# Kernel optimization log

Measured on AMD Instinct MI355X. Metric: run time of the kernel, lower is better.

The kernel has to match this reference:

```python
import jax, jax.numpy as jnp
import numpy as np

N_NODES = 50000
E = 800000
D = 64
H = 128


def _ln(x, g, b, eps=1e-5):
    m = x.mean(-1, keepdims=True)
    v = ((x - m) ** 2).mean(-1, keepdims=True)
    return (x - m) * jax.lax.rsqrt(v + eps) * g + b


def setup_inputs() -> dict:
    key = jax.random.key(0)
    ks = jax.random.split(key, 8)
    return dict(
        node_emb=jax.random.normal(ks[0], (N_NODES, D), jnp.float32),
        src=jax.random.randint(ks[1], (E,), 0, N_NODES),
        dst=jax.random.randint(ks[2], (E,), 0, N_NODES),
        noise=jax.random.uniform(ks[3], (E,), jnp.float32, 1e-6, 1.0 - 1e-6),
        W1=jax.random.normal(ks[4], (2 * D, H), jnp.float32) * 0.05,
        b1=jnp.zeros((H,), jnp.float32),
        g1=jnp.ones((H,), jnp.float32),
        bt1=jnp.zeros((H,), jnp.float32),
        W2=jax.random.normal(ks[5], (H, H // 2), jnp.float32) * 0.05,
        b2=jnp.zeros((H // 2,), jnp.float32),
        g2=jnp.ones((H // 2,), jnp.float32),
        bt2=jnp.zeros((H // 2,), jnp.float32),
        W3=jax.random.normal(ks[6], (H // 2, 1), jnp.float32) * 0.05,
        b3=jnp.zeros((1,), jnp.float32),
    )


def reference(node_emb, src, dst, noise, W1, b1, g1, bt1, W2, b2, g2, bt2, W3, b3):
    # edge gather + concat: [E, 2D]
    edge_emb = jnp.concatenate([node_emb[src], node_emb[dst]], axis=1)
    # edge MLP with LayerNorm + relu (dropout=0 / eval)
    h = jax.nn.relu(_ln(edge_emb @ W1 + b1, g1, bt1))
    h = jax.nn.relu(_ln(h @ W2 + b2, g2, bt2))
    logit = (h @ W3 + b3).reshape(-1)  # [E]
    # concrete gate, bias=0, beta=1.0 (forward default)
    beta = 1.0
    gate = jax.nn.sigmoid((jnp.log(noise) - jnp.log1p(-noise) + logit) / beta)
    # degree norm: out_deg(src)^-1/2 * in_deg(dst)^-1/2, degrees clamped to >=1
    ones = jnp.ones((src.shape[0],), node_emb.dtype)
    out_deg = jnp.maximum(jax.ops.segment_sum(ones, src, num_segments=N_NODES), 1.0)
    in_deg = jnp.maximum(jax.ops.segment_sum(ones, dst, num_segments=N_NODES), 1.0)
    norm = jax.lax.rsqrt(out_deg)[src] * jax.lax.rsqrt(in_deg)[dst]
    return gate * norm
```

## Files before the change

kernel.cpp:

```cpp
#include <hip/hip_runtime.h>
#include <hip/hip_bf16.h>

#define N_NODES 50000
#define NE      800000
#define NT32    (NE / 32)
#define NTILES  (NE / 16)

typedef __attribute__((ext_vector_type(8)))  short bf16x8;
typedef __attribute__((ext_vector_type(4)))  float f32x4;
typedef __attribute__((ext_vector_type(16))) float f32x16;
typedef __attribute__((ext_vector_type(4)))  int   i32x4;
typedef __attribute__((ext_vector_type(2)))  int   i32x2;

static __device__ __forceinline__ short f2bf(float x) {
    union { float f; unsigned u; } v; v.f = x;
    unsigned r = (v.u + 0x7fffu + ((v.u >> 16) & 1u)) >> 16;
    return (short)r;
}
static __device__ __forceinline__ float bflo(unsigned u) {
    union { unsigned u; float f; } v; v.u = u << 16; return v.f;
}
static __device__ __forceinline__ float bfhi(unsigned u) {
    union { unsigned u; float f; } v; v.u = u & 0xffff0000u; return v.f;
}
static __device__ __forceinline__ float bfs(unsigned short u) {
    union { unsigned u; float f; } v; v.u = ((unsigned)u) << 16; return v.f;
}
static __device__ __forceinline__ unsigned pk2bf(float a, float b) {
    union { __hip_bfloat162 h; unsigned u; } v;
    float2 f; f.x = a; f.y = b;
    v.h = __float22bfloat162_rn(f);
    return v.u;
}

#define OFF_W2   32768
#define OFF_B1   49152
#define OFF_B2   49408
#define OFF_GT1  49536
#define OFF_GT2  50048
#define OFF_W3   50304
#define IMG_B    50432
#define IMG_V4   (IMG_B / 16)


__global__ void prep_hist(const float* __restrict__ emb,
                          const int* __restrict__ src, const int* __restrict__ dst,
                          const float* __restrict__ W1, const float* __restrict__ b1,
                          const float* __restrict__ g1, const float* __restrict__ bt1,
                          const float* __restrict__ W2, const float* __restrict__ b2,
                          const float* __restrict__ g2, const float* __restrict__ bt2,
                          const float* __restrict__ W3,
                          ushort* __restrict__ embB, char* __restrict__ img,
                          int* __restrict__ outd, int* __restrict__ ind)
{
    const int i0 = blockIdx.x * 256 + threadIdx.x;
    const int n  = gridDim.x * 256;

    for (int t = i0; t < (N_NODES * 64 / 8); t += n) {
        const f32x4* p = (const f32x4*)(emb + (size_t)t * 8);
        f32x4 a = p[0], b = p[1];
        unsigned u0 = pk2bf(a[0], a[1]);
        unsigned u1 = pk2bf(a[2], a[3]);
        unsigned u2 = pk2bf(b[0], b[1]);
        unsigned u3 = pk2bf(b[2], b[3]);
        i32x4 o = {(int)u0, (int)u1, (int)u2, (int)u3};
        *(i32x4*)(embB + (size_t)t * 8) = o;
    }
    for (int t = i0; t < NE; t += n) {
        atomicAdd(outd + src[t], 1);
        atomicAdd(ind + dst[t], 1);
    }
    ushort* W1f = (ushort*)img;
    for (int t = i0; t < 16384; t += n) {
        int j = t & 7, lane = (t >> 3) & 63, f = t >> 9;
        int mt = f >> 3, ke = f & 7, h = lane >> 5, c = lane & 31;
        W1f[t] = f2bf(W1[(16 * ke + 8 * h + j) * 128 + 32 * mt + c]);
    }
    ushort* W2f = (ushort*)(img + OFF_W2);
    for (int t = i0; t < 8192; t += n) {
        int j = t & 7, lane = (t >> 3) & 63, f = t >> 9;
        int mt = f >> 3, ke = f & 7, h = lane >> 5, c = lane & 31;
        W2f[t] = f2bf(W2[(16 * ke + 8 * h + j) * 64 + 32 * mt + c]);
    }
    if (i0 < 128) ((ushort*)(img + OFF_B1))[i0] = f2bf(b1[i0]);
    if (i0 < 64)  ((ushort*)(img + OFF_B2))[i0] = f2bf(b2[i0]);
    if (i0 < 128) {
        int r4 = i0 & 3, h = (i0 >> 2) & 1, q4 = (i0 >> 3) & 3, mt = i0 >> 5;
        int f = 32 * mt + 8 * q4 + 4 * h + r4;
        ((unsigned*)(img + OFF_GT1))[i0] =
            (unsigned)(ushort)f2bf(g1[f]) | ((unsigned)(ushort)f2bf(bt1[f]) << 16);
    }
    if (i0 < 64) {
        int r4 = i0 & 3, h = (i0 >> 2) & 1, q4 = (i0 >> 3) & 3, mt = i0 >> 5;
        int f = 32 * mt + 8 * q4 + 4 * h + r4;
        ((unsigned*)(img + OFF_GT2))[i0] =
            (unsigned)(ushort)f2bf(g2[f]) | ((unsigned)(ushort)f2bf(bt2[f]) << 16);
        ((ushort*)(img + OFF_W3))[i0] = f2bf(W3[f]);
    }
}


__global__ __launch_bounds__(256, 3) void edge_mlp32(
    const ushort* __restrict__ embB,
    const int*   __restrict__ src, const int* __restrict__ dst,
    const float* __restrict__ noise,
    const i32x4* __restrict__ WFimg,
    const float* __restrict__ b3p,
    const int* __restrict__ outd, const int* __restrict__ ind,
    float* __restrict__ out)
{
    __shared__ i32x4 ldsv[IMG_V4];
    char* ldsb = (char*)ldsv;

    const int tid = threadIdx.x;
    for (int i = tid; i < IMG_V4; i += 256) ldsv[i] = WFimg[i];
    __syncthreads();

    const int l   = tid & 63;
    const int h   = l >> 5;
    const int c   = l & 31;

    const float b3v = b3p[0];

    bf16x8 bone = {};
    bone[0] = (h == 0) ? (short)0x3F80 : (short)0;

    const int gw = blockIdx.x * 4 + (tid >> 6);
    const int nw = gridDim.x * 4;

    int sn, dn;
    bf16x8 fA0, fA1, fA2, fA3;
    {
        int t0 = (gw < NT32) ? gw : (NT32 - 1);
        int e0p = t0 * 32 + c;
        sn = src[e0p]; dn = dst[e0p];
        const ushort* sp = embB + (size_t)sn * 64;
        fA0 = *(const bf16x8*)(sp + 8 * h);
        fA1 = *(const bf16x8*)(sp + 16 + 8 * h);
        fA2 = *(const bf16x8*)(sp + 32 + 8 * h);
        fA3 = *(const bf16x8*)(sp + 48 + 8 * h);
    }

    for (int tile = gw; tile < NT32; tile += nw) {
        unsigned tz;
        asm volatile("v_mov_b32 %0, 0" : "=v"(tz));
        const char* ldz = ldsb + tz;

        const int e0 = tile * 32 + c;

        const ushort* dp = embB + (size_t)dn * 64;
        bf16x8 fD0 = *(const bf16x8*)(dp + 8 * h);
        bf16x8 fD1 = *(const bf16x8*)(dp + 16 + 8 * h);
        bf16x8 fD2 = *(const bf16x8*)(dp + 32 + 8 * h);
        bf16x8 fD3 = *(const bf16x8*)(dp + 48 + 8 * h);

        const int tn  = tile + nw;
        const int tcl = (tn < NT32) ? tn : tile;
        const int e0n = tcl * 32 + c;
        int snN = src[e0n];
        int dnN = dst[e0n];
        float nz = noise[e0];
        int odv = outd[sn];
        int idv = ind[dn];

        const ushort* W1z = (const ushort*)ldz;
        f32x16 acc[4] = {};
#pragma unroll
        for (int ke = 0; ke < 4; ++ke) {
            bf16x8 bf = (ke == 0) ? fA0 : (ke == 1) ? fA1 : (ke == 2) ? fA2 : fA3;
#pragma unroll
            for (int mt = 0; mt < 4; ++mt) {
                bf16x8 w = *(const bf16x8*)(W1z + (mt * 8 + ke) * 512 + l * 8);
                acc[mt] = __builtin_amdgcn_mfma_f32_32x32x16_bf16(w, bf, acc[mt], 0, 0, 0);
            }
        }
#pragma unroll
        for (int ke = 4; ke < 8; ++ke) {
            bf16x8 bf = (ke == 4) ? fD0 : (ke == 5) ? fD1 : (ke == 6) ? fD2 : fD3;
#pragma unroll
            for (int mt = 0; mt < 4; ++mt) {
                bf16x8 w = *(const bf16x8*)(W1z + (mt * 8 + ke) * 512 + l * 8);
                acc[mt] = __builtin_amdgcn_mfma_f32_32x32x16_bf16(w, bf, acc[mt], 0, 0, 0);
            }
        }
        const ushort* b1z = (const ushort*)(ldz + OFF_B1);
#pragma unroll
        for (int mt = 0; mt < 4; ++mt) {
            bf16x8 w = {};
            short bv = b1z[32 * mt + c];
            w[0] = (h == 0) ? bv : (short)0;
            acc[mt] = __builtin_amdgcn_mfma_f32_32x32x16_bf16(w, bone, acc[mt], 0, 0, 0);
        }

        float s0 = 0.f, s1 = 0.f, q0 = 0.f, q1 = 0.f;
#pragma unroll
        for (int mt = 0; mt < 4; ++mt) {
#pragma unroll
            for (int i = 0; i < 16; i += 2) {
                float v0 = acc[mt][i], v1 = acc[mt][i + 1];
                s0 += v0; q0 = fmaf(v0, v0, q0);
                s1 += v1; q1 = fmaf(v1, v1, q1);
            }
        }
        float s = s0 + s1, q = q0 + q1;
        s += __shfl_xor(s, 32);
        q += __shfl_xor(q, 32);
        const float mu = s * (1.0f / 128.0f);
        const float rs = rsqrtf(q * (1.0f / 128.0f) - mu * mu + 1e-5f);
        const float c0 = -mu * rs;

        const ushort* W2z = (const ushort*)(ldz + OFF_W2);
        f32x16 acc2[2] = {};
#pragma unroll
        for (int mt = 0; mt < 4; ++mt) {
            unsigned pk[4][2];
#pragma unroll
            for (int q4 = 0; q4 < 4; ++q4) {
                i32x4 pg = *(const i32x4*)(ldz + OFF_GT1 + ((mt * 4 + q4) * 2 + h) * 16);
                float t[4];
#pragma unroll
                for (int r4 = 0; r4 < 4; ++r4) {
                    unsigned u = (unsigned)pg[r4];
                    float v = acc[mt][q4 * 4 + r4];
                    float w = fmaf(v, rs, c0);
                    float y = fmaf(w, bflo(u), bfhi(u));
                    t[r4] = fmaxf(y, 0.f);
                }
                pk[q4][0] = pk2bf(t[0], t[1]);
                pk[q4][1] = pk2bf(t[2], t[3]);
            }
#pragma unroll
            for (int sub = 0; sub < 2; ++sub) {
                const int ke = 2 * mt + sub;
                const int qa = 2 * sub, qb = qa + 1;
                unsigned S0 = h ? pk[qa][0] : pk[qb][0];
                unsigned S1 = h ? pk[qa][1] : pk[qb][1];
                unsigned r0 = (unsigned)__shfl_xor((int)S0, 32);
                unsigned r1 = (unsigned)__shfl_xor((int)S1, 32);
                unsigned o0 = h ? pk[qb][0] : pk[qa][0];
                unsigned o1 = h ? pk[qb][1] : pk[qa][1];
                union { i32x4 i; bf16x8 b; } u;
                u.i[0] = (int)(h ? r0 : o0);
                u.i[1] = (int)(h ? r1 : o1);
                u.i[2] = (int)(h ? o0 : r0);
                u.i[3] = (int)(h ? o1 : r1);
#pragma unroll
                for (int mt2 = 0; mt2 < 2; ++mt2) {
                    bf16x8 w = *(const bf16x8*)(W2z + (mt2 * 8 + ke) * 512 + l * 8);
                    acc2[mt2] = __builtin_amdgcn_mfma_f32_32x32x16_bf16(w, u.b, acc2[mt2], 0, 0, 0);
                }
            }
        }
        const ushort* b2z = (const ushort*)(ldz + OFF_B2);
#pragma unroll
        for (int mt2 = 0; mt2 < 2; ++mt2) {
            bf16x8 w = {};
            short bv = b2z[32 * mt2 + c];
            w[0] = (h == 0) ? bv : (short)0;
            acc2[mt2] = __builtin_amdgcn_mfma_f32_32x32x16_bf16(w, bone, acc2[mt2], 0, 0, 0);
        }

        {
            const ushort* spn = embB + (size_t)snN * 64;
            fA0 = *(const bf16x8*)(spn + 8 * h);
            fA1 = *(const bf16x8*)(spn + 16 + 8 * h);
            fA2 = *(const bf16x8*)(spn + 32 + 8 * h);
            fA3 = *(const bf16x8*)(spn + 48 + 8 * h);
        }

        float t0 = 0.f, t1 = 0.f, p0 = 0.f, p1 = 0.f;
#pragma unroll
        for (int mt2 = 0; mt2 < 2; ++mt2) {
#pragma unroll
            for (int i = 0; i < 16; i += 2) {
                float v0 = acc2[mt2][i], v1 = acc2[mt2][i + 1];
                t0 += v0; p0 = fmaf(v0, v0, p0);
                t1 += v1; p1 = fmaf(v1, v1, p1);
            }
        }
        float s2 = t0 + t1, q2 = p0 + p1;
        s2 += __shfl_xor(s2, 32);
        q2 += __shfl_xor(q2, 32);
        const float mu2 = s2 * (1.0f / 64.0f);
        const float rs2 = rsqrtf(q2 * (1.0f / 64.0f) - mu2 * mu2 + 1e-5f);
        const float c02 = -mu2 * rs2;

        float lg = 0.f;
#pragma unroll
        for (int mt2 = 0; mt2 < 2; ++mt2) {
#pragma unroll
            for (int q4 = 0; q4 < 4; ++q4) {
                const int bse = (mt2 * 4 + q4) * 2 + h;
                i32x4 pg = *(const i32x4*)(ldz + OFF_GT2 + bse * 16);
                i32x2 wq = *(const i32x2*)(ldz + OFF_W3 + bse * 8);
#pragma unroll
                for (int r4 = 0; r4 < 4; ++r4) {
                    unsigned ug = (unsigned)pg[r4];
                    unsigned short uw = (unsigned short)(((unsigned)wq[r4 >> 1]) >> (16 * (r4 & 1)));
                    float v = acc2[mt2][q4 * 4 + r4];
                    float w = fmaf(v, rs2, c02);
                    float y = fmaf(w, bflo(ug), bfhi(ug));
                    y = fmaxf(y, 0.f);
                    lg = fmaf(y, bfs(uw), lg);
                }
            }
        }
        lg += __shfl_xor(lg, 32);
        lg += b3v;

        if (h == 0) {
            float z = __logf(nz) - log1pf(-nz) + lg;
            float gate = 1.0f / (1.0f + __expf(-z));
            int od = odv; if (od < 1) od = 1;
            int idg = idv; if (idg < 1) idg = 1;
            out[e0] = gate * (rsqrtf((float)od) * rsqrtf((float)idg));
        }

        sn = snN; dn = dnN;
    }
}


__global__ void degree_hist(const int* __restrict__ src, const int* __restrict__ dst,
                            int* __restrict__ outd, int* __restrict__ ind) {
    int i = blockIdx.x * 256 + threadIdx.x;
    if (i < NE) {
        atomicAdd(outd + src[i], 1);
        atomicAdd(ind + dst[i], 1);
    }
}

__global__ __launch_bounds__(256, 2) void edge_mlp_mfma(
    const float* __restrict__ emb,
    const int*   __restrict__ src, const int* __restrict__ dst,
    const float* __restrict__ noise,
    const float* __restrict__ W1, const float* __restrict__ b1,
    const float* __restrict__ g1, const float* __restrict__ bt1,
    const float* __restrict__ W2, const float* __restrict__ b2,
    const float* __restrict__ g2, const float* __restrict__ bt2,
    const float* __restrict__ W3, const float* __restrict__ b3,
    const int*   __restrict__ outd, const int* __restrict__ ind,
    float* __restrict__ out)
{
    __shared__ short lds[32768];
    const int tid = threadIdx.x;
    const int wid = tid >> 6;
    const int l   = tid & 63;
    const int g   = l >> 4;
    const int c   = l & 15;

    for (int i = tid; i < 16384; i += 256) {
        int j = i & 7, lane = (i >> 3) & 63, p = i >> 9;
        int ks = p >> 3, t = p & 7;
        int row = ks * 32 + (lane >> 4) * 8 + j;
        int col = t * 16 + (lane & 15);
        lds[i] = f2bf(W1[row * 128 + col]);
    }
    for (int i = tid; i < 8192; i += 256) {
        int j = i & 7, lane = (i >> 3) & 63, p = i >> 9;
        int ks = p >> 2, t = p & 3;
        int row = ks * 32 + (lane >> 4) * 8 + j;
        int col = t * 16 + (lane & 15);
        lds[16384 + i] = f2bf(W2[row * 64 + col]);
    }
    __syncthreads();

    short* Hl = lds + 24576 + wid * 2048;
    float b1v[8], g1v[8], t1v[8];
#pragma unroll
    for (int t = 0; t < 8; ++t) { int f = t * 16 + c; b1v[t] = b1[f]; g1v[t] = g1[f]; t1v[t] = bt1[f]; }
    float b2v[4], g2v[4], t2v[4], w3v[4];
#pragma unroll
    for (int t = 0; t < 4; ++t) { int f = t * 16 + c; b2v[t] = b2[f]; g2v[t] = g2[f]; t2v[t] = bt2[f]; w3v[t] = W3[f]; }
    const float b3v = b3[0];

    const int gw = blockIdx.x * 4 + wid;
    const int nw = gridDim.x * 4;

    for (int tile = gw; tile < NTILES; tile += nw) {
        const int e0 = tile * 16 + c;
        const int sn = src[e0], dn = dst[e0];
        const f32x4* sp = (const f32x4*)(emb + (size_t)sn * 64);
        const f32x4* dp = (const f32x4*)(emb + (size_t)dn * 64);
        f32x4 u[8];
        u[0] = sp[2 * g]; u[1] = sp[2 * g + 1];
        u[2] = sp[8 + 2 * g]; u[3] = sp[8 + 2 * g + 1];
        u[4] = dp[2 * g]; u[5] = dp[2 * g + 1];
        u[6] = dp[8 + 2 * g]; u[7] = dp[8 + 2 * g + 1];

        bf16x8 a1[4];
#pragma unroll
        for (int ks = 0; ks < 4; ++ks) {
            f32x4 x0 = u[2 * ks], x1 = u[2 * ks + 1];
            bf16x8 a;
            a[0] = f2bf(x0[0]); a[1] = f2bf(x0[1]); a[2] = f2bf(x0[2]); a[3] = f2bf(x0[3]);
            a[4] = f2bf(x1[0]); a[5] = f2bf(x1[1]); a[6] = f2bf(x1[2]); a[7] = f2bf(x1[3]);
            a1[ks] = a;
        }
        f32x4 acc1[8];
#pragma unroll
        for (int t = 0; t < 8; ++t) { f32x4 z = {b1v[t], b1v[t], b1v[t], b1v[t]}; acc1[t] = z; }
#pragma unroll
        for (int ks = 0; ks < 4; ++ks) {
#pragma unroll
            for (int t = 0; t < 8; ++t) {
                bf16x8 b = *(const bf16x8*)(lds + (ks * 8 + t) * 512 + l * 8);
                acc1[t] = __builtin_amdgcn_mfma_f32_16x16x32_bf16(a1[ks], b, acc1[t], 0, 0, 0);
            }
        }
        float mean[4], rstd[4];
#pragma unroll
        for (int r = 0; r < 4; ++r) {
            float s = acc1[0][r];
#pragma unroll
            for (int t = 1; t < 8; ++t) s += acc1[t][r];
            s += __shfl_xor(s, 1); s += __shfl_xor(s, 2);
            s += __shfl_xor(s, 4); s += __shfl_xor(s, 8);
            float m = s * (1.0f / 128.0f);
            float q = 0.f;
#pragma unroll
            for (int t = 0; t < 8; ++t) { float d = acc1[t][r] - m; q = fmaf(d, d, q); }
            q += __shfl_xor(q, 1); q += __shfl_xor(q, 2);
            q += __shfl_xor(q, 4); q += __shfl_xor(q, 8);
            mean[r] = m; rstd[r] = rsqrtf(q * (1.0f / 128.0f) + 1e-5f);
        }
#pragma unroll
        for (int r = 0; r < 4; ++r) {
            int rw = g * 4 + r;
            int swz = (rw & 7) << 3;
#pragma unroll
            for (int t = 0; t < 8; ++t) {
                float y = fmaf((acc1[t][r] - mean[r]) * rstd[r], g1v[t], t1v[t]);
                y = fmaxf(y, 0.f);
                Hl[rw * 128 + ((t * 16 + c) ^ swz)] = f2bf(y);
            }
        }
        bf16x8 a2[4];
        const int swzr = (c & 7) << 3;
#pragma unroll
        for (int ks = 0; ks < 4; ++ks)
            a2[ks] = *(const bf16x8*)(Hl + c * 128 + ((ks * 32 + g * 8) ^ swzr));

        f32x4 acc2[4];
#pragma unroll
        for (int t = 0; t < 4; ++t) { f32x4 z = {b2v[t], b2v[t], b2v[t], b2v[t]}; acc2[t] = z; }
#pragma unroll
        for (int ks = 0; ks < 4; ++ks) {
#pragma unroll
            for (int t = 0; t < 4; ++t) {
                bf16x8 b = *(const bf16x8*)(lds + 16384 + (ks * 4 + t) * 512 + l * 8);
                acc2[t] = __builtin_amdgcn_mfma_f32_16x16x32_bf16(a2[ks], b, acc2[t], 0, 0, 0);
            }
        }
        float logit[4];
#pragma unroll
        for (int r = 0; r < 4; ++r) {
            float s = acc2[0][r] + acc2[1][r] + acc2[2][r] + acc2[3][r];
            s += __shfl_xor(s, 1); s += __shfl_xor(s, 2);
            s += __shfl_xor(s, 4); s += __shfl_xor(s, 8);
            float m = s * (1.0f / 64.0f);
            float q = 0.f;
#pragma unroll
            for (int t = 0; t < 4; ++t) { float d = acc2[t][r] - m; q = fmaf(d, d, q); }
            q += __shfl_xor(q, 1); q += __shfl_xor(q, 2);
            q += __shfl_xor(q, 4); q += __shfl_xor(q, 8);
            float rs = rsqrtf(q * (1.0f / 64.0f) + 1e-5f);
            float p = 0.f;
#pragma unroll
            for (int t = 0; t < 4; ++t) {
                float y = fmaf((acc2[t][r] - m) * rs, g2v[t], t2v[t]);
                y = fmaxf(y, 0.f);
                p = fmaf(y, w3v[t], p);
            }
            p += __shfl_xor(p, 1); p += __shfl_xor(p, 2);
            p += __shfl_xor(p, 4); p += __shfl_xor(p, 8);
            logit[r] = p + b3v;
        }
        if (c < 4) {
            int e = tile * 16 + g * 4 + c;
            float lg = (c == 0) ? logit[0] : (c == 1) ? logit[1] : (c == 2) ? logit[2] : logit[3];
            float nz = noise[e];
            float z = __logf(nz) - log1pf(-nz) + lg;
            float gate = 1.0f / (1.0f + __expf(-z));
            int od = outd[src[e]]; if (od < 1) od = 1;
            int idg = ind[dst[e]]; if (idg < 1) idg = 1;
            out[e] = gate * (rsqrtf((float)od) * rsqrtf((float)idg));
        }
    }
}


extern "C" void kernel_launch(void* const* d_in, const int* in_sizes, int n_in,
                              void* d_out, int out_size, void* d_ws, size_t ws_size,
                              hipStream_t stream) {
    const float* emb   = (const float*)d_in[0];
    const int*   src   = (const int*)  d_in[1];
    const int*   dst   = (const int*)  d_in[2];
    const float* noise = (const float*)d_in[3];
    const float* W1  = (const float*)d_in[4];
    const float* b1  = (const float*)d_in[5];
    const float* g1  = (const float*)d_in[6];
    const float* bt1 = (const float*)d_in[7];
    const float* W2  = (const float*)d_in[8];
    const float* b2  = (const float*)d_in[9];
    const float* g2  = (const float*)d_in[10];
    const float* bt2 = (const float*)d_in[11];
    const float* W3  = (const float*)d_in[12];
    const float* b3  = (const float*)d_in[13];

    char* ws = (char*)d_ws;
    const size_t NEED = 6400000 + IMG_B + 400000;

    if (ws_size >= NEED) {
        ushort* embB = (ushort*)ws;
        char*   img  = ws + 6400000;
        int* outd = (int*)(ws + 6400000 + IMG_B);
        int* ind  = outd + N_NODES;

        hipMemsetAsync(outd, 0, 2 * N_NODES * sizeof(int), stream);
        prep_hist<<<2048, 256, 0, stream>>>(emb, src, dst, W1, b1, g1, bt1,
                                            W2, b2, g2, bt2, W3,
                                            embB, img, outd, ind);
        edge_mlp32<<<768, 256, 0, stream>>>(embB, src, dst, noise, (const i32x4*)img,
                                            b3, outd, ind, (float*)d_out);
    } else {
        int* outd = (int*)ws;
        int* ind  = outd + N_NODES;
        hipMemsetAsync(outd, 0, 2 * N_NODES * sizeof(int), stream);
        degree_hist<<<(NE + 255) / 256, 256, 0, stream>>>(src, dst, outd, ind);
        edge_mlp_mfma<<<512, 256, 0, stream>>>(emb, src, dst, noise,
                                               W1, b1, g1, bt1,
                                               W2, b2, g2, bt2,
                                               W3, b3, outd, ind,
                                               (float*)d_out);
    }
}
```

Measured before the change: 150.4 us.

## Compute layer-1 MFMA in two halves, keep bf16 activations, defer scalar loads

Splits the first-layer MFMA accumulation into two passes of two 32-column tiles and packs each result to bf16 right away. Only 8 packed VGPRs per tile stay live instead of four full f32x16 accumulators, which cuts register pressure and could allow higher occupancy. The next-tile src/dst prefetch and the noise/degree loads move after the LayerNorm statistics and go through an opaque zero offset so the compiler cannot hoist them back. The degree-counting atomics also now read src/dst four at a time with vector loads. In exchange, the LayerNorm input is rounded to bf16 before normalization, which adds a small precision loss.

```diff
diff --git a/kernel.cpp b/kernel.cpp
--- a/kernel.cpp
+++ b/kernel.cpp
@@ -66,9 +66,13 @@
         i32x4 o = {(int)u0, (int)u1, (int)u2, (int)u3};
         *(i32x4*)(embB + (size_t)t * 8) = o;
     }
-    for (int t = i0; t < NE; t += n) {
-        atomicAdd(outd + src[t], 1);
-        atomicAdd(ind + dst[t], 1);
+    for (int t = i0; t < NE / 4; t += n) {
+        i32x4 s4 = ((const i32x4*)src)[t];
+        i32x4 d4 = ((const i32x4*)dst)[t];
+        atomicAdd(outd + s4[0], 1); atomicAdd(outd + s4[1], 1);
+        atomicAdd(outd + s4[2], 1); atomicAdd(outd + s4[3], 1);
+        atomicAdd(ind + d4[0], 1); atomicAdd(ind + d4[1], 1);
+        atomicAdd(ind + d4[2], 1); atomicAdd(ind + d4[3], 1);
     }
     ushort* W1f = (ushort*)img;
     for (int t = i0; t < 16384; t += n) {
@@ -154,52 +158,47 @@
         bf16x8 fD2 = *(const bf16x8*)(dp + 32 + 8 * h);
         bf16x8 fD3 = *(const bf16x8*)(dp + 48 + 8 * h);
 
-        const int tn  = tile + nw;
-        const int tcl = (tn < NT32) ? tn : tile;
-        const int e0n = tcl * 32 + c;
-        int snN = src[e0n];
-        int dnN = dst[e0n];
-        float nz = noise[e0];
-        int odv = outd[sn];
-        int idv = ind[dn];
-
         const ushort* W1z = (const ushort*)ldz;
-        f32x16 acc[4] = {};
-#pragma unroll
-        for (int ke = 0; ke < 4; ++ke) {
-            bf16x8 bf = (ke == 0) ? fA0 : (ke == 1) ? fA1 : (ke == 2) ? fA2 : fA3;
-#pragma unroll
-            for (int mt = 0; mt < 4; ++mt) {
-                bf16x8 w = *(const bf16x8*)(W1z + (mt * 8 + ke) * 512 + l * 8);
-                acc[mt] = __builtin_amdgcn_mfma_f32_32x32x16_bf16(w, bf, acc[mt], 0, 0, 0);
-            }
-        }
-#pragma unroll
-        for (int ke = 4; ke < 8; ++ke) {
-            bf16x8 bf = (ke == 4) ? fD0 : (ke == 5) ? fD1 : (ke == 6) ? fD2 : fD3;
-#pragma unroll
-            for (int mt = 0; mt < 4; ++mt) {
-                bf16x8 w = *(const bf16x8*)(W1z + (mt * 8 + ke) * 512 + l * 8);
-                acc[mt] = __builtin_amdgcn_mfma_f32_32x32x16_bf16(w, bf, acc[mt], 0, 0, 0);
-            }
-        }
         const ushort* b1z = (const ushort*)(ldz + OFF_B1);
-#pragma unroll
-        for (int mt = 0; mt < 4; ++mt) {
-            bf16x8 w = {};
-            short bv = b1z[32 * mt + c];
-            w[0] = (h == 0) ? bv : (short)0;
-            acc[mt] = __builtin_amdgcn_mfma_f32_32x32x16_bf16(w, bone, acc[mt], 0, 0, 0);
-        }
-
+        unsigned pkh[4][4][2];
         float s0 = 0.f, s1 = 0.f, q0 = 0.f, q1 = 0.f;
 #pragma unroll
-        for (int mt = 0; mt < 4; ++mt) {
-#pragma unroll
-            for (int i = 0; i < 16; i += 2) {
-                float v0 = acc[mt][i], v1 = acc[mt][i + 1];
-                s0 += v0; q0 = fmaf(v0, v0, q0);
-                s1 += v1; q1 = fmaf(v1, v1, q1);
+        for (int mp = 0; mp < 2; ++mp) {
+            f32x16 a0 = {}, a1 = {};
+#pragma unroll
+            for (int ke = 0; ke < 8; ++ke) {
+                bf16x8 bf = (ke == 0) ? fA0 : (ke == 1) ? fA1 : (ke == 2) ? fA2 :
+                            (ke == 3) ? fA3 : (ke == 4) ? fD0 : (ke == 5) ? fD1 :
+                            (ke == 6) ? fD2 : fD3;
+                bf16x8 w0 = *(const bf16x8*)(W1z + ((2 * mp) * 8 + ke) * 512 + l * 8);
+                a0 = __builtin_amdgcn_mfma_f32_32x32x16_bf16(w0, bf, a0, 0, 0, 0);
+                bf16x8 w1 = *(const bf16x8*)(W1z + ((2 * mp + 1) * 8 + ke) * 512 + l * 8);
+                a1 = __builtin_amdgcn_mfma_f32_32x32x16_bf16(w1, bf, a1, 0, 0, 0);
+            }
+            {
+                bf16x8 w = {};
+                short bv = b1z[32 * (2 * mp) + c];
+                w[0] = (h == 0) ? bv : (short)0;
+                a0 = __builtin_amdgcn_mfma_f32_32x32x16_bf16(w, bone, a0, 0, 0, 0);
+                bf16x8 w2_ = {};
+                short bv1 = b1z[32 * (2 * mp + 1) + c];
+                w2_[0] = (h == 0) ? bv1 : (short)0;
+                a1 = __builtin_amdgcn_mfma_f32_32x32x16_bf16(w2_, bone, a1, 0, 0, 0);
+            }
+#pragma unroll
+            for (int q4 = 0; q4 < 4; ++q4) {
+                float v0 = a0[4 * q4],     v1 = a0[4 * q4 + 1];
+                float v2 = a0[4 * q4 + 2], v3 = a0[4 * q4 + 3];
+                s0 += v0 + v2; q0 = fmaf(v0, v0, fmaf(v2, v2, q0));
+                s1 += v1 + v3; q1 = fmaf(v1, v1, fmaf(v3, v3, q1));
+                pkh[2 * mp][q4][0] = pk2bf(v0, v1);
+                pkh[2 * mp][q4][1] = pk2bf(v2, v3);
+                float u0 = a1[4 * q4],     u1 = a1[4 * q4 + 1];
+                float u2 = a1[4 * q4 + 2], u3 = a1[4 * q4 + 3];
+                s0 += u0 + u2; q0 = fmaf(u0, u0, fmaf(u2, u2, q0));
+                s1 += u1 + u3; q1 = fmaf(u1, u1, fmaf(u3, u3, q1));
+                pkh[2 * mp + 1][q4][0] = pk2bf(u0, u1);
+                pkh[2 * mp + 1][q4][1] = pk2bf(u2, u3);
             }
         }
         float s = s0 + s1, q = q0 + q1;
@@ -209,6 +208,22 @@
         const float rs = rsqrtf(q * (1.0f / 128.0f) - mu * mu + 1e-5f);
         const float c0 = -mu * rs;
 
+        unsigned tz2;
+        asm volatile("v_mov_b32 %0, 0" : "=v"(tz2));
+        const int tn  = tile + nw;
+        const int tcl = (tn < NT32) ? tn : tile;
+        const int e0n = tcl * 32 + c;
+        const int*   srcx = (const int*)((const char*)src + tz2);
+        const int*   dstx = (const int*)((const char*)dst + tz2);
+        const float* noix = (const float*)((const char*)noise + tz2);
+        const int*   outx = (const int*)((const char*)outd + tz2);
+        const int*   indx = (const int*)((const char*)ind + tz2);
+        int snN = srcx[e0n];
+        int dnN = dstx[e0n];
+        float nz = noix[e0];
+        int odv = outx[sn];
+        int idv = indx[dn];
+
         const ushort* W2z = (const ushort*)(ldz + OFF_W2);
         f32x16 acc2[2] = {};
 #pragma unroll
@@ -220,8 +235,9 @@
                 float t[4];
 #pragma unroll
                 for (int r4 = 0; r4 < 4; ++r4) {
+                    unsigned hv = pkh[mt][q4][r4 >> 1];
+                    float v = (r4 & 1) ? bfhi(hv) : bflo(hv);
                     unsigned u = (unsigned)pg[r4];
-                    float v = acc[mt][q4 * 4 + r4];
                     float w = fmaf(v, rs, c0);
                     float y = fmaf(w, bflo(u), bfhi(u));
                     t[r4] = fmaxf(y, 0.f);
```

Result: slower. 161.6 us (+7.4%).

## Deepen gather prefetch pipeline to full next tile and vectorize degree histogram

Applied to the files above, without the earlier changes.

The edge MLP kernel now prefetches both source and destination embedding rows for the next tile at the start of each iteration, and the edge indices two tiles ahead. Previously only the source rows were prefetched and the destination gather stalled the current tile. This raises register pressure, so launch bounds drop to 2 waves per SIMD and the grid shrinks to 512 blocks. The histogram loop in prep also reads src and dst as int4 vectors to cut the number of load instructions.

```diff
diff --git a/kernel.cpp b/kernel.cpp
--- a/kernel.cpp
+++ b/kernel.cpp
@@ -66,9 +66,13 @@
         i32x4 o = {(int)u0, (int)u1, (int)u2, (int)u3};
         *(i32x4*)(embB + (size_t)t * 8) = o;
     }
-    for (int t = i0; t < NE; t += n) {
-        atomicAdd(outd + src[t], 1);
-        atomicAdd(ind + dst[t], 1);
+    for (int t = i0; t < NE / 4; t += n) {
+        i32x4 s4 = ((const i32x4*)src)[t];
+        i32x4 d4 = ((const i32x4*)dst)[t];
+        atomicAdd(outd + s4[0], 1); atomicAdd(outd + s4[1], 1);
+        atomicAdd(outd + s4[2], 1); atomicAdd(outd + s4[3], 1);
+        atomicAdd(ind + d4[0], 1); atomicAdd(ind + d4[1], 1);
+        atomicAdd(ind + d4[2], 1); atomicAdd(ind + d4[3], 1);
     }
     ushort* W1f = (ushort*)img;
     for (int t = i0; t < 16384; t += n) {
@@ -100,7 +104,7 @@
 }
 
 
-__global__ __launch_bounds__(256, 3) void edge_mlp32(
+__global__ __launch_bounds__(256, 2) void edge_mlp32(
     const ushort* __restrict__ embB,
     const int*   __restrict__ src, const int* __restrict__ dst,
     const float* __restrict__ noise,
@@ -128,17 +132,25 @@
     const int gw = blockIdx.x * 4 + (tid >> 6);
     const int nw = gridDim.x * 4;
 
-    int sn, dn;
-    bf16x8 fA0, fA1, fA2, fA3;
+    int sn, dn, snN, dnN;
+    bf16x8 fA0, fA1, fA2, fA3, fD0, fD1, fD2, fD3;
     {
         int t0 = (gw < NT32) ? gw : (NT32 - 1);
         int e0p = t0 * 32 + c;
         sn = src[e0p]; dn = dst[e0p];
         const ushort* sp = embB + (size_t)sn * 64;
+        const ushort* dp = embB + (size_t)dn * 64;
         fA0 = *(const bf16x8*)(sp + 8 * h);
         fA1 = *(const bf16x8*)(sp + 16 + 8 * h);
         fA2 = *(const bf16x8*)(sp + 32 + 8 * h);
         fA3 = *(const bf16x8*)(sp + 48 + 8 * h);
+        fD0 = *(const bf16x8*)(dp + 8 * h);
+        fD1 = *(const bf16x8*)(dp + 16 + 8 * h);
+        fD2 = *(const bf16x8*)(dp + 32 + 8 * h);
+        fD3 = *(const bf16x8*)(dp + 48 + 8 * h);
+        int t1 = t0 + nw; int t1c = (t1 < NT32) ? t1 : t0;
+        int e1p = t1c * 32 + c;
+        snN = src[e1p]; dnN = dst[e1p];
     }
 
     for (int tile = gw; tile < NT32; tile += nw) {
@@ -148,17 +160,24 @@
 
         const int e0 = tile * 32 + c;
 
-        const ushort* dp = embB + (size_t)dn * 64;
-        bf16x8 fD0 = *(const bf16x8*)(dp + 8 * h);
-        bf16x8 fD1 = *(const bf16x8*)(dp + 16 + 8 * h);
-        bf16x8 fD2 = *(const bf16x8*)(dp + 32 + 8 * h);
-        bf16x8 fD3 = *(const bf16x8*)(dp + 48 + 8 * h);
-
-        const int tn  = tile + nw;
-        const int tcl = (tn < NT32) ? tn : tile;
-        const int e0n = tcl * 32 + c;
-        int snN = src[e0n];
-        int dnN = dst[e0n];
+        bf16x8 nA0, nA1, nA2, nA3, nD0, nD1, nD2, nD3;
+        {
+            const ushort* spn = embB + (size_t)snN * 64;
+            const ushort* dpn = embB + (size_t)dnN * 64;
+            nA0 = *(const bf16x8*)(spn + 8 * h);
+            nA1 = *(const bf16x8*)(spn + 16 + 8 * h);
+            nA2 = *(const bf16x8*)(spn + 32 + 8 * h);
+            nA3 = *(const bf16x8*)(spn + 48 + 8 * h);
+            nD0 = *(const bf16x8*)(dpn + 8 * h);
+            nD1 = *(const bf16x8*)(dpn + 16 + 8 * h);
+            nD2 = *(const bf16x8*)(dpn + 32 + 8 * h);
+            nD3 = *(const bf16x8*)(dpn + 48 + 8 * h);
+        }
+        const int tnn = tile + 2 * nw;
+        const int tcc = (tnn < NT32) ? tnn : tile;
+        const int enn = tcc * 32 + c;
+        int snNN = src[enn];
+        int dnNN = dst[enn];
         float nz = noise[e0];
         int odv = outd[sn];
         int idv = ind[dn];
@@ -260,14 +279,6 @@
             acc2[mt2] = __builtin_amdgcn_mfma_f32_32x32x16_bf16(w, bone, acc2[mt2], 0, 0, 0);
         }
 
-        {
-            const ushort* spn = embB + (size_t)snN * 64;
-            fA0 = *(const bf16x8*)(spn + 8 * h);
-            fA1 = *(const bf16x8*)(spn + 16 + 8 * h);
-            fA2 = *(const bf16x8*)(spn + 32 + 8 * h);
-            fA3 = *(const bf16x8*)(spn + 48 + 8 * h);
-        }
-
         float t0 = 0.f, t1 = 0.f, p0 = 0.f, p1 = 0.f;
 #pragma unroll
         for (int mt2 = 0; mt2 < 2; ++mt2) {
@@ -316,7 +327,9 @@
             out[e0] = gate * (rsqrtf((float)od) * rsqrtf((float)idg));
         }
 
-        sn = snN; dn = dnN;
+        fA0 = nA0; fA1 = nA1; fA2 = nA2; fA3 = nA3;
+        fD0 = nD0; fD1 = nD1; fD2 = nD2; fD3 = nD3;
+        sn = snN; dn = dnN; snN = snNN; dnN = dnNN;
     }
 }
 
@@ -521,7 +534,7 @@
         prep_hist<<<2048, 256, 0, stream>>>(emb, src, dst, W1, b1, g1, bt1,
                                             W2, b2, g2, bt2, W3,
                                             embB, img, outd, ind);
-        edge_mlp32<<<768, 256, 0, stream>>>(embB, src, dst, noise, (const i32x4*)img,
+        edge_mlp32<<<512, 256, 0, stream>>>(embB, src, dst, noise, (const i32x4*)img,
                                             b3, outd, ind, (float*)d_out);
     } else {
         int* outd = (int*)ws;
```

Result: slower. 158.3 us (+5.3%).
